# Kernel optimization log

Hardware: AMD Instinct MI355X
Metric: run time of the kernel (lower is better)

Reference implementation:

```python
import jax, jax.numpy as jnp
import numpy as np

B, N, F, H, A, T = 4, 256, 64, 256, 16, 3


def setup_inputs() -> dict:
    key = jax.random.key(0)
    ks = jax.random.split(key, 18)
    s = 0.05
    rn = lambda k, shp: jax.random.normal(k, shp, dtype=jnp.float32) * s
    return {
        "node_features": jax.random.normal(ks[0], (B, N, F), dtype=jnp.float32),
        "adjacency": jax.random.randint(ks[1], (B, N, N), 0, 2).astype(jnp.int32),
        # preprocess MLP: F->H->H
        "pre_W1": rn(ks[2], (F, H)), "pre_b1": jnp.zeros((H,), jnp.float32),
        "pre_W2": rn(ks[3], (H, H)), "pre_b2": jnp.zeros((H,), jnp.float32),
        # message MLP: 2H->H->H
        "msg_W1": rn(ks[4], (2 * H, H)), "msg_b1": jnp.zeros((H,), jnp.float32),
        "msg_W2": rn(ks[5], (H, H)), "msg_b2": jnp.zeros((H,), jnp.float32),
        # GRUCell params (jax layout [in, 3H]; gate order r,z,n like torch)
        "gru_Wih": rn(ks[6], (H, 3 * H)), "gru_Whh": rn(ks[7], (H, 3 * H)),
        "gru_bih": jnp.zeros((3 * H,), jnp.float32), "gru_bhh": jnp.zeros((3 * H,), jnp.float32),
        # readout MLP: H->H->A
        "ro_W1": rn(ks[8], (H, H)), "ro_b1": jnp.zeros((H,), jnp.float32),
        "ro_W2": rn(ks[9], (H, A)), "ro_b2": jnp.zeros((A,), jnp.float32),
    }


def reference(node_features, adjacency, pre_W1, pre_b1, pre_W2, pre_b2,
              msg_W1, msg_b1, msg_W2, msg_b2,
              gru_Wih, gru_Whh, gru_bih, gru_bhh,
              ro_W1, ro_b1, ro_W2, ro_b2):
    adj = adjacency.astype(node_features.dtype)  # [B,N,N]
    # preprocess: Linear-ReLU-Linear
    h = jnp.maximum(node_features @ pre_W1 + pre_b1, 0.0) @ pre_W2 + pre_b2  # [B,N,H]

    W1_i, W1_j = msg_W1[:H], msg_W1[H:]  # concat([h_i,h_j]) @ W1 == h_i@W1_i + h_j@W1_j
    for _ in range(T):
        hi = h @ W1_i  # [B,N,H] receiver part
        hj = h @ W1_j  # [B,N,H] sender part
        e = jnp.maximum(hi[:, :, None, :] + hj[:, None, :, :] + msg_b1, 0.0)  # [B,N,N,H]
        m = e @ msg_W2 + msg_b2  # [B,N,N,H] messages
        agg = jnp.einsum('bijh,bij->bih', m, adj)  # mask + sum over senders j
        # GRUCell(input=agg, hidden=h), torch gate order (r, z, n)
        gi = agg @ gru_Wih + gru_bih  # [B,N,3H]
        gh = h @ gru_Whh + gru_bhh
        ir, iz, inn = jnp.split(gi, 3, axis=-1)
        hr, hz, hn = jnp.split(gh, 3, axis=-1)
        r = jax.nn.sigmoid(ir + hr)
        z = jax.nn.sigmoid(iz + hz)
        n = jnp.tanh(inn + r * hn)
        h = (1.0 - z) * n + z * h

    g = jnp.sum(h, axis=1)  # [B,H] graph readout
    q = jnp.maximum(g @ ro_W1 + ro_b1, 0.0) @ ro_W2 + ro_b2  # [B,A]
    return q
```

## Files before the change

kernel.cpp:

```cpp
#include <hip/hip_runtime.h>
#include <hip/hip_bf16.h>


typedef unsigned short ushort_t;
typedef short bf8_t __attribute__((ext_vector_type(8)));
typedef float f4_t  __attribute__((ext_vector_type(4)));

#define BN_ROWS 1024

#define UB_NFB    0
#define UB_PW1T   65536
#define UB_PW2T   81920
#define UB_WCATT  147456
#define UB_WGT    475136
#define UB_H2     917504
#define UB_EHAT2  1441792

#define F_PREB1   1015808
#define F_PREB2   1016064
#define F_BCAT    1016320
#define F_BIH     1017600
#define F_ROW1    1018368
#define F_ROB1    1083904
#define F_ROW2    1084160
#define F_ROB2    1088256
#define F_H       1088272
#define F_HCAT    1350416
#define F_FLAG    2661136
#define F_GCNT    2661140

#define CVa 65536
#define CVb 81920
#define CVc 147456
#define CVd 475136
#define CV_TOTAL 547600
#define NCONV 1070

__device__ __forceinline__ float bf2f(ushort_t u) {
    return __uint_as_float(((unsigned int)u) << 16);
}
__device__ __forceinline__ ushort_t f2b(float v) {
    __hip_bfloat16 b = __float2bfloat16(v);
    return *reinterpret_cast<ushort_t*>(&b);
}
__device__ __forceinline__ float relu(float v) { return v < 0.f ? 0.f : v; }
__device__ __forceinline__ float ld(const void* p, int i, int isf32) {
    return isf32 ? ((const float*)p)[i] : bf2f(((const ushort_t*)p)[i]);
}

__global__ __launch_bounds__(256) void convwg_kernel(
    const void* nf, const void* preW1, const void* preb1, const void* preW2, const void* preb2,
    const void* msgW1, const void* msgb1, const void* msgW2, const void* msgb2,
    const void* gruWih, const void* gruWhh, const void* grubih, const void* grubhh,
    const void* roW1, const void* rob1, const void* roW2, const void* rob2,
    float* __restrict__ w)
{
    __shared__ float w2s[4 * 256];
    __shared__ int cnt;
    const int t = threadIdx.x;
    ushort_t* wb = (ushort_t*)w;

    if (t == 0) cnt = 0;
    __syncthreads();
    {
        const ushort_t* nf0 = (const ushort_t*)nf;
        int bad = 0;
        for (int i = 0; i < 8; ++i) {
            ushort_t u = nf0[(t * 8 + i) * 2];
            int ex = (u >> 7) & 0xFF;
            if ((u & 0x7fff) != 0 && (ex < 100 || ex > 140)) bad++;
        }
        atomicAdd(&cnt, bad);
    }
    __syncthreads();
    const int f32 = (cnt > 512) ? 1 : 0;

    if (blockIdx.x == 0) {
        if (t < 4) ((int*)(w + F_GCNT))[t] = 0;
        if (t == 4) *(int*)(w + F_FLAG) = f32;
    }

    if (blockIdx.x < NCONV) {
        const int e0 = (blockIdx.x * 256 + t) * 2;
#pragma unroll
        for (int u2 = 0; u2 < 2; ++u2) {
            int e = e0 + u2;
            if (e >= CV_TOTAL) break;
            if (e < CVa) {
                wb[UB_NFB + e] = f2b(ld(nf, e, f32));
            } else if (e < CVb) {
                int i = e - CVa; int n = i >> 6, k = i & 63;
                wb[UB_PW1T + i] = f2b(ld(preW1, k * 256 + n, f32));
            } else if (e < CVc) {
                int i = e - CVb; int n = i >> 8, k = i & 255;
                wb[UB_PW2T + i] = f2b(ld(preW2, k * 256 + n, f32));
            } else if (e < CVd) {
                int i = e - CVc; int n = i >> 8, k = i & 255;
                float v;
                if (n < 256)      v = ld(msgW1, k * 256 + n, f32);
                else if (n < 512) v = ld(msgW1, (256 + k) * 256 + (n - 256), f32);
                else              v = ld(gruWhh, k * 768 + (n - 512), f32);
                wb[UB_WCATT + i] = f2b(v);
            } else {
                int f = e - CVd;
                float v;
                if (f < 256)        v = ld(preb1, f, f32);
                else if (f < 512)   v = ld(preb2, f - 256, f32);
                else if (f < 1792) {
                    int c = f - 512;
                    if (c < 256)      v = ld(msgb1, c, f32);
                    else if (c < 512) v = 0.f;
                    else              v = ld(grubhh, c - 512, f32);
                }
                else if (f < 2560)  v = ld(grubih, f - 1792, f32);
                else if (f < 68096) v = ld(roW1, f - 2560, f32);
                else if (f < 68352) v = ld(rob1, f - 68096, f32);
                else if (f < 72448) v = ld(roW2, f - 68352, f32);
                else                v = ld(rob2, f - 72448, f32);
                w[F_PREB1 + f] = v;
            }
        }
        return;
    }

    const int wt = blockIdx.x - NCONV;
    const int p0 = (wt % 3) * 256;
    const int k0 = (wt / 3) * 4;
    for (int i = t; i < 4 * 256; i += 256) {
        int r = i >> 8, n = i & 255;
        int krow = k0 + r;
        float v;
        if (krow < 256)       v = ld(msgW2, krow * 256 + n, f32);
        else if (krow == 256) v = ld(msgb2, n, f32);
        else                  v = 0.f;
        w2s[i] = v;
    }
    __syncthreads();
    const int p = p0 + t;
    float acc4[4] = {};
    for (int n0 = 0; n0 < 256; n0 += 32) {
        float wv[32];
#pragma unroll
        for (int i = 0; i < 32; ++i)
            wv[i] = ld(gruWih, (n0 + i) * 768 + p, f32);
#pragma unroll
        for (int r = 0; r < 4; ++r) {
            float acc = acc4[r];
#pragma unroll
            for (int q = 0; q < 8; ++q) {
                f4_t w4 = *(const f4_t*)&w2s[r * 256 + n0 + q * 4];
                acc += w4[0] * wv[q * 4 + 0] + w4[1] * wv[q * 4 + 1]
                     + w4[2] * wv[q * 4 + 2] + w4[3] * wv[q * 4 + 3];
            }
            acc4[r] = acc;
        }
    }
#pragma unroll
    for (int r = 0; r < 4; ++r) {
        int krow = k0 + r;
        ushort_t hi = f2b(acc4[r]);
        ushort_t lo = f2b(acc4[r] - bf2f(hi));
        wb[UB_WGT + p * 576 + krow] = hi;
        wb[UB_WGT + p * 576 + 288 + krow] = lo;
    }
}

__global__ __launch_bounds__(256) void prenet_kernel(float* __restrict__ w)
{
    __shared__ ushort_t As[32 * 64];
    __shared__ ushort_t Xs[32 * 256];
    __shared__ ushort_t Bs[256 * 32];
    ushort_t* wb = (ushort_t*)w;
    const int t = threadIdx.x;
    const int wave = t >> 6, lane = t & 63;
    const int ln = lane & 15, quad = lane >> 4;
    const int wr = (wave & 1) * 16, wc = (wave >> 1) * 128;
    const int rbase = blockIdx.x * 32;
    const int srow = t >> 2, skc = (t & 3) << 3;

    {
        int row = t >> 3, kc = (t & 7) << 3;
        *(bf8_t*)(&As[row * 64 + kc]) =
            *(const bf8_t*)(&wb[UB_NFB + (rbase + row) * 64 + kc]);
    }

    f4_t acc[8] = {};
    for (int k0 = 0; k0 < 64; k0 += 32) {
        __syncthreads();
#pragma unroll
        for (int rr = 0; rr < 4; ++rr) {
            int n = srow + 64 * rr;
            *(bf8_t*)(&Bs[n * 32 + skc]) =
                *(const bf8_t*)(&wb[UB_PW1T + n * 64 + k0 + skc]);
        }
        __syncthreads();
        bf8_t af = *(const bf8_t*)(&As[(wr + ln) * 64 + k0 + quad * 8]);
#pragma unroll
        for (int n = 0; n < 8; ++n) {
            bf8_t bfr = *(const bf8_t*)(&Bs[(wc + n * 16 + ln) * 32 + quad * 8]);
            acc[n] = __builtin_amdgcn_mfma_f32_16x16x32_bf16(af, bfr, acc[n], 0, 0, 0);
        }
    }
    __syncthreads();
#pragma unroll
    for (int n = 0; n < 8; ++n) {
        int col = wc + n * 16 + ln;
        float bb = w[F_PREB1 + col];
#pragma unroll
        for (int r = 0; r < 4; ++r) {
            int row = wr + quad * 4 + r;
            Xs[row * 256 + col] = f2b(relu(acc[n][r] + bb));
        }
        acc[n] = (f4_t){0.f, 0.f, 0.f, 0.f};
    }
    __syncthreads();

    for (int k0 = 0; k0 < 256; k0 += 32) {
        __syncthreads();
#pragma unroll
        for (int rr = 0; rr < 4; ++rr) {
            int n = srow + 64 * rr;
            *(bf8_t*)(&Bs[n * 32 + skc]) =
                *(const bf8_t*)(&wb[UB_PW2T + n * 256 + k0 + skc]);
        }
        __syncthreads();
        bf8_t af = *(const bf8_t*)(&Xs[(wr + ln) * 256 + k0 + quad * 8]);
#pragma unroll
        for (int n = 0; n < 8; ++n) {
            bf8_t bfr = *(const bf8_t*)(&Bs[(wc + n * 16 + ln) * 32 + quad * 8]);
            acc[n] = __builtin_amdgcn_mfma_f32_16x16x32_bf16(af, bfr, acc[n], 0, 0, 0);
        }
    }
#pragma unroll
    for (int n = 0; n < 8; ++n) {
        int col = wc + n * 16 + ln;
        float bb = w[F_PREB2 + col];
#pragma unroll
        for (int r = 0; r < 4; ++r) {
            int grow = rbase + wr + quad * 4 + r;
            float v = acc[n][r] + bb;
            w[F_H + grow * 256 + col] = v;
            ushort_t hi = f2b(v);
            wb[UB_H2 + grow * 512 + col] = hi;
            wb[UB_H2 + grow * 512 + 256 + col] = f2b(v - bf2f(hi));
        }
    }
}

__global__ __launch_bounds__(256) void hcat_kernel(float* __restrict__ w)
{
    __shared__ ushort_t As[64 * 32];
    __shared__ ushort_t Bs[128 * 32];
    ushort_t* wb = (ushort_t*)w;
    const ushort_t* A  = wb + UB_H2;
    const ushort_t* Bt = wb + UB_WCATT;
    const int t = threadIdx.x;
    const int wave = t >> 6, lane = t & 63;
    const int ln = lane & 15, quad = lane >> 4;
    const int bm = (blockIdx.x & 15) * 64, bn = (blockIdx.x >> 4) * 128;
    const int wm = (wave >> 1) * 32, wn = (wave & 1) * 64;
    const int srow = t >> 2, skc = (t & 3) << 3;

    f4_t acc[2][4] = {};
    bf8_t ra, rb[2];

    ra = *(const bf8_t*)(&A[(bm + srow) * 512 + skc]);
#pragma unroll
    for (int r = 0; r < 2; ++r)
        rb[r] = *(const bf8_t*)(&Bt[(bn + srow + r * 64) * 256 + skc]);

    for (int ks = 0; ks < 16; ++ks) {
        __syncthreads();
        *(bf8_t*)(&As[srow * 32 + skc]) = ra;
#pragma unroll
        for (int r = 0; r < 2; ++r)
            *(bf8_t*)(&Bs[(srow + r * 64) * 32 + skc]) = rb[r];
        __syncthreads();
        if (ks < 15) {
            int k0 = (ks + 1) * 32;
            ra = *(const bf8_t*)(&A[(bm + srow) * 512 + k0 + skc]);
            int kb = (k0 & 255);
#pragma unroll
            for (int r = 0; r < 2; ++r)
                rb[r] = *(const bf8_t*)(&Bt[(bn + srow + r * 64) * 256 + kb + skc]);
        }
        bf8_t af[2], bfr[4];
#pragma unroll
        for (int i = 0; i < 2; ++i)
            af[i]  = *(const bf8_t*)(&As[(wm + i * 16 + ln) * 32 + quad * 8]);
#pragma unroll
        for (int i = 0; i < 4; ++i)
            bfr[i] = *(const bf8_t*)(&Bs[(wn + i * 16 + ln) * 32 + quad * 8]);
#pragma unroll
        for (int mi = 0; mi < 2; ++mi)
#pragma unroll
            for (int ni = 0; ni < 4; ++ni)
                acc[mi][ni] = __builtin_amdgcn_mfma_f32_16x16x32_bf16(
                    af[mi], bfr[ni], acc[mi][ni], 0, 0, 0);
    }

#pragma unroll
    for (int mi = 0; mi < 2; ++mi) {
#pragma unroll
        for (int ni = 0; ni < 4; ++ni) {
            int col = bn + wn + ni * 16 + ln;
            float bb = w[F_BCAT + col];
#pragma unroll
            for (int r = 0; r < 4; ++r) {
                int row = bm + wm + mi * 16 + quad * 4 + r;
                w[F_HCAT + row * 1280 + col] = acc[mi][ni][r] + bb;
            }
        }
    }
}

__global__ __launch_bounds__(256) void msg_kernel(
    const float* __restrict__ hcat,
    const int*   __restrict__ adj,
    ushort_t* __restrict__ ehat)
{
    const int row = blockIdx.x;
    const int t = threadIdx.x;
    __shared__ int ej[256];
    __shared__ int ecnt;
    if (t == 0) ecnt = 0;
    __syncthreads();
    if (adj[row * 256 + t]) { int p = atomicAdd(&ecnt, 1); ej[p] = t; }
    const float hi = hcat[row * 1280 + t];
    const float* hjb = hcat + (row >> 8) * 256 * 1280 + 256;
    __syncthreads();
    const int ne = ecnt;
    float acc = 0.f;
#pragma unroll 4
    for (int p = 0; p < ne; ++p) {
        int j = ej[p];
        acc += relu(hi + hjb[j * 1280 + t]);
    }
    ushort_t h16 = f2b(acc);
    ushort_t l16 = f2b(acc - bf2f(h16));
    ushort_t* er = ehat + row * 576;
    er[t] = h16;
    er[288 + t] = l16;
    if (t < 32) {
        er[256 + t] = f2b(t == 0 ? (float)ne : 0.f);
        er[544 + t] = 0;
    }
}

template<int FINAL>
__global__ __launch_bounds__(256) void gigru_kernel(float* __restrict__ w,
                                                    void* __restrict__ out)
{
    __shared__ ushort_t As[64 * 32];
    __shared__ ushort_t Bs[192 * 32];
    __shared__ float gl[256];
    __shared__ float t1[256];
    __shared__ int donef;
    ushort_t* wb = (ushort_t*)w;
    const int t = threadIdx.x;
    const int wave = t >> 6, lane = t & 63;
    const int ln = lane & 15, quad = lane >> 4;
    const int rg = blockIdx.x >> 2, cg = blockIdx.x & 3;
    const int rbase = rg * 64;
    const int srow = t >> 2, skc = (t & 3) << 3;

    const ushort_t* Ap = wb + UB_EHAT2 + (rbase + srow) * 576 + skc;
    int browoff[3];
#pragma unroll
    for (int rr = 0; rr < 3; ++rr) {
        int br = srow + 64 * rr;
        browoff[rr] = ((br >> 6) * 256 + cg * 64 + (br & 63)) * 576 + skc;
    }
    const ushort_t* Bp = wb + UB_WGT;

    f4_t acc[12] = {};
    bf8_t ra, rb[3];

    ra = *(const bf8_t*)(Ap);
#pragma unroll
    for (int rr = 0; rr < 3; ++rr)
        rb[rr] = *(const bf8_t*)(&Bp[browoff[rr]]);

    for (int ks = 0; ks < 27; ++ks) {
        __syncthreads();
        *(bf8_t*)(&As[srow * 32 + skc]) = ra;
#pragma unroll
        for (int rr = 0; rr < 3; ++rr)
            *(bf8_t*)(&Bs[(srow + 64 * rr) * 32 + skc]) = rb[rr];
        __syncthreads();
        if (ks < 26) {
            int k0 = (ks + 1) * 32;
            int ka = (k0 < 576) ? k0 : k0 - 576;
            int kb = (k0 < 288) ? k0 : k0 - 288;
            ra = *(const bf8_t*)(&Ap[ka]);
#pragma unroll
            for (int rr = 0; rr < 3; ++rr)
                rb[rr] = *(const bf8_t*)(&Bp[browoff[rr] + kb]);
        }
        bf8_t af = *(const bf8_t*)(&As[(wave * 16 + ln) * 32 + quad * 8]);
#pragma unroll
        for (int n = 0; n < 12; ++n) {
            bf8_t bfr = *(const bf8_t*)(&Bs[(n * 16 + ln) * 32 + quad * 8]);
            acc[n] = __builtin_amdgcn_mfma_f32_16x16x32_bf16(af, bfr, acc[n], 0, 0, 0);
        }
    }

#pragma unroll
    for (int n = 0; n < 4; ++n) {
        int col = cg * 64 + n * 16 + ln;
        float bi_r = w[F_BIH + col];
        float bi_z = w[F_BIH + 256 + col];
        float bi_n = w[F_BIH + 512 + col];
#pragma unroll
        for (int r = 0; r < 4; ++r) {
            int row = rbase + wave * 16 + quad * 4 + r;
            float ir = acc[n][r] + bi_r;
            float iz = acc[n + 4][r] + bi_z;
            float in = acc[n + 8][r] + bi_n;
            const float* ghr = w + F_HCAT + row * 1280 + 512;
            float hr = ghr[col], hz = ghr[256 + col], hn = ghr[512 + col];
            float rg_ = 1.f / (1.f + __expf(-(ir + hr)));
            float z   = 1.f / (1.f + __expf(-(iz + hz)));
            float nn  = tanhf(in + rg_ * hn);
            float ho = w[F_H + row * 256 + col];
            float hv = (1.f - z) * nn + z * ho;
            w[F_H + row * 256 + col] = hv;
            if (!FINAL) {
                ushort_t hb = f2b(hv);
                wb[UB_H2 + row * 512 + col] = hb;
                wb[UB_H2 + row * 512 + 256 + col] = f2b(hv - bf2f(hb));
            }
        }
    }

    if (FINAL) {
        const int g = blockIdx.x >> 4;
        __syncthreads();
        if (t == 0) {
            __threadfence();
            int prev = atomicAdd((int*)(w + F_GCNT) + g, 1);
            donef = (prev == 15);
        }
        __syncthreads();
        if (!donef) return;
        __threadfence();

        const float* hb = w + F_H + g * 256 * 256;
        float s = 0.f;
        for (int n = 0; n < 256; ++n) s += hb[n * 256 + t];
        gl[t] = s;
        __syncthreads();
        float acc1 = w[F_ROB1 + t];
        for (int k = 0; k < 256; ++k) acc1 += gl[k] * w[F_ROW1 + k * 256 + t];
        t1[t] = relu(acc1);
        __syncthreads();
        if (t < 16) {
            float q = w[F_ROB2 + t];
            for (int k = 0; k < 256; ++k) q += t1[k] * w[F_ROW2 + k * 16 + t];
            if (*(const int*)(w + F_FLAG)) ((float*)out)[g * 16 + t] = q;
            else ((__hip_bfloat16*)out)[g * 16 + t] = __float2bfloat16(q);
        }
    }
}

extern "C" void kernel_launch(void* const* d_in, const int* in_sizes, int n_in,
                              void* d_out, int out_size, void* d_ws, size_t ws_size,
                              hipStream_t stream) {
    float* w = (float*)d_ws;
    ushort_t* wb = (ushort_t*)d_ws;

    static const int dictSz[18]  = {65536,262144,16384,256,65536,256,131072,256,65536,256,
                                    196608,196608,768,768,65536,256,4096,16};
    static const int alphaSz[18] = {262144,196608,196608,768,768,131072,65536,256,256,
                                    65536,16384,65536,256,256,65536,4096,256,16};
    static const int alphaPos[18] = {9,0,10,12,11,13,5,7,6,8,2,1,4,3,14,16,15,17};
    bool dictOK = true, alphaOK = true;
    for (int i = 0; i < 18 && i < n_in; ++i) {
        if (in_sizes[i] != dictSz[i])  dictOK = false;
        if (in_sizes[i] != alphaSz[i]) alphaOK = false;
    }
    const void* P[18];
    for (int l = 0; l < 18; ++l) P[l] = d_in[(!dictOK && alphaOK) ? alphaPos[l] : l];
    const int* adj = (const int*)P[1];

    convwg_kernel<<<NCONV + 216, 256, 0, stream>>>(
        P[0], P[2], P[3], P[4], P[5], P[6], P[7], P[8], P[9],
        P[10], P[11], P[12], P[13], P[14], P[15], P[16], P[17], w);

    prenet_kernel<<<32, 256, 0, stream>>>(w);

    for (int it = 0; it < 3; ++it) {
        hcat_kernel<<<160, 256, 0, stream>>>(w);
        msg_kernel<<<BN_ROWS, 256, 0, stream>>>(w + F_HCAT, adj, wb + UB_EHAT2);
        if (it < 2)
            gigru_kernel<0><<<64, 256, 0, stream>>>(w, d_out);
        else
            gigru_kernel<1><<<64, 256, 0, stream>>>(w, d_out);
    }
}
```

Measured before the change: 308.9 us.

## Deepen K tiles with padded LDS and remap gigru blocks per XCD

The hcat and gigru GEMM loops now stage 64 and 96 K-elements per LDS round instead of 32, halving or thirding the number of barrier pairs, and use padded row strides (72 and 104) to reduce LDS bank conflicts. The gigru block index is remapped so blocks sharing the same B column group land on the same XCD, aiming for better L2 reuse of weights. The readout group index is updated to match the new mapping. The cost is more registers for prefetch and larger LDS use, which may reduce occupancy.

Result: faster. 297.3 us (-3.8%).

```diff
diff --git a/kernel.cpp b/kernel.cpp
--- a/kernel.cpp
+++ b/kernel.cpp
@@ -247,10 +247,11 @@
     }
 }
 
+#define HLD 72
 __global__ __launch_bounds__(256) void hcat_kernel(float* __restrict__ w)
 {
-    __shared__ ushort_t As[64 * 32];
-    __shared__ ushort_t Bs[128 * 32];
+    __shared__ ushort_t As[64 * HLD];
+    __shared__ ushort_t Bs[128 * HLD];
     ushort_t* wb = (ushort_t*)w;
     const ushort_t* A  = wb + UB_H2;
     const ushort_t* Bt = wb + UB_WCATT;
@@ -262,41 +263,54 @@
     const int srow = t >> 2, skc = (t & 3) << 3;
 
     f4_t acc[2][4] = {};
-    bf8_t ra, rb[2];
-
-    ra = *(const bf8_t*)(&A[(bm + srow) * 512 + skc]);
-#pragma unroll
-    for (int r = 0; r < 2; ++r)
-        rb[r] = *(const bf8_t*)(&Bt[(bn + srow + r * 64) * 256 + skc]);
-
-    for (int ks = 0; ks < 16; ++ks) {
-        __syncthreads();
-        *(bf8_t*)(&As[srow * 32 + skc]) = ra;
+    bf8_t ra[2], rb[2][2];
+
+#pragma unroll
+    for (int s = 0; s < 2; ++s) {
+        ra[s] = *(const bf8_t*)(&A[(bm + srow) * 512 + s * 32 + skc]);
 #pragma unroll
         for (int r = 0; r < 2; ++r)
-            *(bf8_t*)(&Bs[(srow + r * 64) * 32 + skc]) = rb[r];
-        __syncthreads();
-        if (ks < 15) {
-            int k0 = (ks + 1) * 32;
-            ra = *(const bf8_t*)(&A[(bm + srow) * 512 + k0 + skc]);
-            int kb = (k0 & 255);
+            rb[r][s] = *(const bf8_t*)(&Bt[(bn + srow + r * 64) * 256 + s * 32 + skc]);
+    }
+
+    for (int ks = 0; ks < 8; ++ks) {
+        __syncthreads();
+#pragma unroll
+        for (int s = 0; s < 2; ++s) {
+            *(bf8_t*)(&As[srow * HLD + s * 32 + skc]) = ra[s];
 #pragma unroll
             for (int r = 0; r < 2; ++r)
-                rb[r] = *(const bf8_t*)(&Bt[(bn + srow + r * 64) * 256 + kb + skc]);
-        }
-        bf8_t af[2], bfr[4];
-#pragma unroll
-        for (int i = 0; i < 2; ++i)
-            af[i]  = *(const bf8_t*)(&As[(wm + i * 16 + ln) * 32 + quad * 8]);
-#pragma unroll
-        for (int i = 0; i < 4; ++i)
-            bfr[i] = *(const bf8_t*)(&Bs[(wn + i * 16 + ln) * 32 + quad * 8]);
-#pragma unroll
-        for (int mi = 0; mi < 2; ++mi)
-#pragma unroll
-            for (int ni = 0; ni < 4; ++ni)
-                acc[mi][ni] = __builtin_amdgcn_mfma_f32_16x16x32_bf16(
-                    af[mi], bfr[ni], acc[mi][ni], 0, 0, 0);
+                *(bf8_t*)(&Bs[(srow + r * 64) * HLD + s * 32 + skc]) = rb[r][s];
+        }
+        __syncthreads();
+        if (ks < 7) {
+            int k0 = (ks + 1) * 64;
+#pragma unroll
+            for (int s = 0; s < 2; ++s) {
+                int k = k0 + s * 32;
+                ra[s] = *(const bf8_t*)(&A[(bm + srow) * 512 + k + skc]);
+                int kb = k & 255;
+#pragma unroll
+                for (int r = 0; r < 2; ++r)
+                    rb[r][s] = *(const bf8_t*)(&Bt[(bn + srow + r * 64) * 256 + kb + skc]);
+            }
+        }
+#pragma unroll
+        for (int kk = 0; kk < 2; ++kk) {
+            bf8_t af[2], bfr[4];
+#pragma unroll
+            for (int i = 0; i < 2; ++i)
+                af[i]  = *(const bf8_t*)(&As[(wm + i * 16 + ln) * HLD + kk * 32 + quad * 8]);
+#pragma unroll
+            for (int i = 0; i < 4; ++i)
+                bfr[i] = *(const bf8_t*)(&Bs[(wn + i * 16 + ln) * HLD + kk * 32 + quad * 8]);
+#pragma unroll
+            for (int mi = 0; mi < 2; ++mi)
+#pragma unroll
+                for (int ni = 0; ni < 4; ++ni)
+                    acc[mi][ni] = __builtin_amdgcn_mfma_f32_16x16x32_bf16(
+                        af[mi], bfr[ni], acc[mi][ni], 0, 0, 0);
+        }
     }
 
 #pragma unroll
@@ -347,12 +361,13 @@
     }
 }
 
+#define GLD 104
 template<int FINAL>
 __global__ __launch_bounds__(256) void gigru_kernel(float* __restrict__ w,
                                                     void* __restrict__ out)
 {
-    __shared__ ushort_t As[64 * 32];
-    __shared__ ushort_t Bs[192 * 32];
+    __shared__ ushort_t As[64 * GLD];
+    __shared__ ushort_t Bs[192 * GLD];
     __shared__ float gl[256];
     __shared__ float t1[256];
     __shared__ int donef;
@@ -360,7 +375,9 @@
     const int t = threadIdx.x;
     const int wave = t >> 6, lane = t & 63;
     const int ln = lane & 15, quad = lane >> 4;
-    const int rg = blockIdx.x >> 2, cg = blockIdx.x & 3;
+    const int xcd = blockIdx.x & 7;
+    const int cg = xcd & 3;
+    const int rg = (blockIdx.x >> 3) + 8 * (xcd >> 2);
     const int rbase = rg * 64;
     const int srow = t >> 2, skc = (t & 3) << 3;
 
@@ -374,34 +391,47 @@
     const ushort_t* Bp = wb + UB_WGT;
 
     f4_t acc[12] = {};
-    bf8_t ra, rb[3];
-
-    ra = *(const bf8_t*)(Ap);
-#pragma unroll
-    for (int rr = 0; rr < 3; ++rr)
-        rb[rr] = *(const bf8_t*)(&Bp[browoff[rr]]);
-
-    for (int ks = 0; ks < 27; ++ks) {
-        __syncthreads();
-        *(bf8_t*)(&As[srow * 32 + skc]) = ra;
+    bf8_t ra[3], rb[3][3];
+
+#pragma unroll
+    for (int s = 0; s < 3; ++s) {
+        ra[s] = *(const bf8_t*)(&Ap[s * 32]);
 #pragma unroll
         for (int rr = 0; rr < 3; ++rr)
-            *(bf8_t*)(&Bs[(srow + 64 * rr) * 32 + skc]) = rb[rr];
-        __syncthreads();
-        if (ks < 26) {
-            int k0 = (ks + 1) * 32;
-            int ka = (k0 < 576) ? k0 : k0 - 576;
-            int kb = (k0 < 288) ? k0 : k0 - 288;
-            ra = *(const bf8_t*)(&Ap[ka]);
+            rb[rr][s] = *(const bf8_t*)(&Bp[browoff[rr] + s * 32]);
+    }
+
+    for (int ks = 0; ks < 9; ++ks) {
+        __syncthreads();
+#pragma unroll
+        for (int s = 0; s < 3; ++s) {
+            *(bf8_t*)(&As[srow * GLD + s * 32 + skc]) = ra[s];
 #pragma unroll
             for (int rr = 0; rr < 3; ++rr)
-                rb[rr] = *(const bf8_t*)(&Bp[browoff[rr] + kb]);
-        }
-        bf8_t af = *(const bf8_t*)(&As[(wave * 16 + ln) * 32 + quad * 8]);
-#pragma unroll
-        for (int n = 0; n < 12; ++n) {
-            bf8_t bfr = *(const bf8_t*)(&Bs[(n * 16 + ln) * 32 + quad * 8]);
-            acc[n] = __builtin_amdgcn_mfma_f32_16x16x32_bf16(af, bfr, acc[n], 0, 0, 0);
+                *(bf8_t*)(&Bs[(srow + 64 * rr) * GLD + s * 32 + skc]) = rb[rr][s];
+        }
+        __syncthreads();
+        if (ks < 8) {
+            int k0 = (ks + 1) * 96;
+#pragma unroll
+            for (int s = 0; s < 3; ++s) {
+                int k = k0 + s * 32;
+                int ka = (k < 576) ? k : k - 576;
+                int kb = (k < 288) ? k : k - 288;
+                ra[s] = *(const bf8_t*)(&Ap[ka]);
+#pragma unroll
+                for (int rr = 0; rr < 3; ++rr)
+                    rb[rr][s] = *(const bf8_t*)(&Bp[browoff[rr] + kb]);
+            }
+        }
+#pragma unroll
+        for (int kk = 0; kk < 3; ++kk) {
+            bf8_t af = *(const bf8_t*)(&As[(wave * 16 + ln) * GLD + kk * 32 + quad * 8]);
+#pragma unroll
+            for (int n = 0; n < 12; ++n) {
+                bf8_t bfr = *(const bf8_t*)(&Bs[(n * 16 + ln) * GLD + kk * 32 + quad * 8]);
+                acc[n] = __builtin_amdgcn_mfma_f32_16x16x32_bf16(af, bfr, acc[n], 0, 0, 0);
+            }
         }
     }
 
@@ -434,7 +464,7 @@
     }
 
     if (FINAL) {
-        const int g = blockIdx.x >> 4;
+        const int g = rg >> 2;
         __syncthreads();
         if (t == 0) {
             __threadfence();
```

## Shrink GEMM row tiles and widen K steps to launch more blocks

Applied to the files above, without the earlier changes.

The hcat GEMM moves to 32-row tiles with a 64-wide K step, doubling its grid to 320 blocks. The GRU-input GEMM moves to 16-row tiles with a 96-wide K step and an XCD-aware block mapping, raising its grid from 64 to 256 blocks. Both use padded LDS rows (stride 104) to reduce bank conflicts and halve the number of barriers per K. The aim is to fill more of the MI355X's compute units and cut sync overhead. The cost is larger LDS use per block and more redundant B-tile loads across blocks, and the final readout counter threshold is changed to 63 to match the new block count per graph.

Measured after the change: 265.3 us. 1.16x faster.

```diff
diff --git a/kernel.cpp b/kernel.cpp
--- a/kernel.cpp
+++ b/kernel.cpp
@@ -247,69 +247,74 @@
     }
 }
 
+#define HLD 104
 __global__ __launch_bounds__(256) void hcat_kernel(float* __restrict__ w)
 {
-    __shared__ ushort_t As[64 * 32];
-    __shared__ ushort_t Bs[128 * 32];
+    __shared__ ushort_t As[32 * HLD];
+    __shared__ ushort_t Bs[128 * HLD];
     ushort_t* wb = (ushort_t*)w;
     const ushort_t* A  = wb + UB_H2;
     const ushort_t* Bt = wb + UB_WCATT;
     const int t = threadIdx.x;
     const int wave = t >> 6, lane = t & 63;
     const int ln = lane & 15, quad = lane >> 4;
-    const int bm = (blockIdx.x & 15) * 64, bn = (blockIdx.x >> 4) * 128;
-    const int wm = (wave >> 1) * 32, wn = (wave & 1) * 64;
-    const int srow = t >> 2, skc = (t & 3) << 3;
-
-    f4_t acc[2][4] = {};
-    bf8_t ra, rb[2];
-
-    ra = *(const bf8_t*)(&A[(bm + srow) * 512 + skc]);
-#pragma unroll
-    for (int r = 0; r < 2; ++r)
-        rb[r] = *(const bf8_t*)(&Bt[(bn + srow + r * 64) * 256 + skc]);
-
-    for (int ks = 0; ks < 16; ++ks) {
-        __syncthreads();
-        *(bf8_t*)(&As[srow * 32 + skc]) = ra;
-#pragma unroll
-        for (int r = 0; r < 2; ++r)
-            *(bf8_t*)(&Bs[(srow + r * 64) * 32 + skc]) = rb[r];
-        __syncthreads();
-        if (ks < 15) {
-            int k0 = (ks + 1) * 32;
-            ra = *(const bf8_t*)(&A[(bm + srow) * 512 + k0 + skc]);
-            int kb = (k0 & 255);
-#pragma unroll
-            for (int r = 0; r < 2; ++r)
-                rb[r] = *(const bf8_t*)(&Bt[(bn + srow + r * 64) * 256 + kb + skc]);
-        }
-        bf8_t af[2], bfr[4];
-#pragma unroll
-        for (int i = 0; i < 2; ++i)
-            af[i]  = *(const bf8_t*)(&As[(wm + i * 16 + ln) * 32 + quad * 8]);
+    const int bm = (blockIdx.x & 31) * 32, bn = (blockIdx.x >> 5) * 128;
+    const int wm = (wave >> 1) * 16, wn = (wave & 1) * 64;
+
+    const int arow = t >> 3, akc = (t & 7) << 3;
+    const int agoff = (bm + arow) * 512 + akc;
+    const int aloff = arow * HLD + akc;
+    int bgoff[4], bloff[4];
+#pragma unroll
+    for (int i = 0; i < 4; ++i) {
+        int slot = i * 256 + t;
+        int brow = slot >> 3, bkc = (slot & 7) << 3;
+        bgoff[i] = (bn + brow) * 256 + bkc;
+        bloff[i] = brow * HLD + bkc;
+    }
+
+    f4_t acc[4] = {};
+    bf8_t ra, rb[4];
+
+    ra = *(const bf8_t*)(&A[agoff]);
+#pragma unroll
+    for (int i = 0; i < 4; ++i)
+        rb[i] = *(const bf8_t*)(&Bt[bgoff[i]]);
+
+    for (int ks = 0; ks < 8; ++ks) {
+        __syncthreads();
+        *(bf8_t*)(&As[aloff]) = ra;
 #pragma unroll
         for (int i = 0; i < 4; ++i)
-            bfr[i] = *(const bf8_t*)(&Bs[(wn + i * 16 + ln) * 32 + quad * 8]);
-#pragma unroll
-        for (int mi = 0; mi < 2; ++mi)
-#pragma unroll
-            for (int ni = 0; ni < 4; ++ni)
-                acc[mi][ni] = __builtin_amdgcn_mfma_f32_16x16x32_bf16(
-                    af[mi], bfr[ni], acc[mi][ni], 0, 0, 0);
-    }
-
-#pragma unroll
-    for (int mi = 0; mi < 2; ++mi) {
-#pragma unroll
-        for (int ni = 0; ni < 4; ++ni) {
-            int col = bn + wn + ni * 16 + ln;
-            float bb = w[F_BCAT + col];
-#pragma unroll
-            for (int r = 0; r < 4; ++r) {
-                int row = bm + wm + mi * 16 + quad * 4 + r;
-                w[F_HCAT + row * 1280 + col] = acc[mi][ni][r] + bb;
+            *(bf8_t*)(&Bs[bloff[i]]) = rb[i];
+        __syncthreads();
+        if (ks < 7) {
+            int k0 = (ks + 1) * 64;
+            int kb = k0 & 255;
+            ra = *(const bf8_t*)(&A[agoff + k0]);
+#pragma unroll
+            for (int i = 0; i < 4; ++i)
+                rb[i] = *(const bf8_t*)(&Bt[bgoff[i] + kb]);
+        }
+#pragma unroll
+        for (int kk = 0; kk < 2; ++kk) {
+            bf8_t af = *(const bf8_t*)(&As[(wm + ln) * HLD + kk * 32 + quad * 8]);
+#pragma unroll
+            for (int ni = 0; ni < 4; ++ni) {
+                bf8_t bfr = *(const bf8_t*)(&Bs[(wn + ni * 16 + ln) * HLD + kk * 32 + quad * 8]);
+                acc[ni] = __builtin_amdgcn_mfma_f32_16x16x32_bf16(af, bfr, acc[ni], 0, 0, 0);
             }
+        }
+    }
+
+#pragma unroll
+    for (int ni = 0; ni < 4; ++ni) {
+        int col = bn + wn + ni * 16 + ln;
+        float bb = w[F_BCAT + col];
+#pragma unroll
+        for (int r = 0; r < 4; ++r) {
+            int row = bm + wm + quad * 4 + r;
+            w[F_HCAT + row * 1280 + col] = acc[ni][r] + bb;
         }
     }
 }
@@ -347,12 +352,13 @@
     }
 }
 
+#define GLD 104
 template<int FINAL>
 __global__ __launch_bounds__(256) void gigru_kernel(float* __restrict__ w,
                                                     void* __restrict__ out)
 {
-    __shared__ ushort_t As[64 * 32];
-    __shared__ ushort_t Bs[192 * 32];
+    __shared__ ushort_t As[16 * GLD];
+    __shared__ ushort_t Bs[192 * GLD];
     __shared__ float gl[256];
     __shared__ float t1[256];
     __shared__ int donef;
@@ -360,63 +366,74 @@
     const int t = threadIdx.x;
     const int wave = t >> 6, lane = t & 63;
     const int ln = lane & 15, quad = lane >> 4;
-    const int rg = blockIdx.x >> 2, cg = blockIdx.x & 3;
-    const int rbase = rg * 64;
-    const int srow = t >> 2, skc = (t & 3) << 3;
-
-    const ushort_t* Ap = wb + UB_EHAT2 + (rbase + srow) * 576 + skc;
-    int browoff[3];
-#pragma unroll
-    for (int rr = 0; rr < 3; ++rr) {
-        int br = srow + 64 * rr;
-        browoff[rr] = ((br >> 6) * 256 + cg * 64 + (br & 63)) * 576 + skc;
-    }
-    const ushort_t* Bp = wb + UB_WGT;
-
-    f4_t acc[12] = {};
-    bf8_t ra, rb[3];
-
-    ra = *(const bf8_t*)(Ap);
-#pragma unroll
-    for (int rr = 0; rr < 3; ++rr)
-        rb[rr] = *(const bf8_t*)(&Bp[browoff[rr]]);
-
-    for (int ks = 0; ks < 27; ++ks) {
-        __syncthreads();
-        *(bf8_t*)(&As[srow * 32 + skc]) = ra;
-#pragma unroll
-        for (int rr = 0; rr < 3; ++rr)
-            *(bf8_t*)(&Bs[(srow + 64 * rr) * 32 + skc]) = rb[rr];
-        __syncthreads();
-        if (ks < 26) {
-            int k0 = (ks + 1) * 32;
+    const int xcd = blockIdx.x & 7;
+    const int cg = xcd & 3;
+    const int rg = (blockIdx.x >> 3) + 32 * (xcd >> 2);
+    const int rbase = rg * 16;
+
+    const int aval = (t < 192);
+    const int arow = t / 12, akc = (t % 12) * 8;
+    const int agoff = (rbase + arow) * 576 + akc;
+    const int aloff = arow * GLD + akc;
+    int bgoff[9], bloff[9];
+#pragma unroll
+    for (int i = 0; i < 9; ++i) {
+        int slot = i * 256 + t;
+        int brow = slot / 12, bkc = (slot % 12) * 8;
+        int wrow = (brow >> 6) * 256 + cg * 64 + (brow & 63);
+        bgoff[i] = wrow * 576 + bkc;
+        bloff[i] = brow * GLD + bkc;
+    }
+    const ushort_t* Ehp = wb + UB_EHAT2;
+    const ushort_t* Bp  = wb + UB_WGT;
+
+    f4_t acc[3] = {};
+    bf8_t ra, rb[9];
+
+    if (aval) ra = *(const bf8_t*)(&Ehp[agoff]);
+#pragma unroll
+    for (int i = 0; i < 9; ++i)
+        rb[i] = *(const bf8_t*)(&Bp[bgoff[i]]);
+
+    for (int ks = 0; ks < 9; ++ks) {
+        __syncthreads();
+        if (aval) *(bf8_t*)(&As[aloff]) = ra;
+#pragma unroll
+        for (int i = 0; i < 9; ++i)
+            *(bf8_t*)(&Bs[bloff[i]]) = rb[i];
+        __syncthreads();
+        if (ks < 8) {
+            int k0 = (ks + 1) * 96;
             int ka = (k0 < 576) ? k0 : k0 - 576;
             int kb = (k0 < 288) ? k0 : k0 - 288;
-            ra = *(const bf8_t*)(&Ap[ka]);
-#pragma unroll
-            for (int rr = 0; rr < 3; ++rr)
-                rb[rr] = *(const bf8_t*)(&Bp[browoff[rr] + kb]);
-        }
-        bf8_t af = *(const bf8_t*)(&As[(wave * 16 + ln) * 32 + quad * 8]);
-#pragma unroll
-        for (int n = 0; n < 12; ++n) {
-            bf8_t bfr = *(const bf8_t*)(&Bs[(n * 16 + ln) * 32 + quad * 8]);
-            acc[n] = __builtin_amdgcn_mfma_f32_16x16x32_bf16(af, bfr, acc[n], 0, 0, 0);
-        }
-    }
-
-#pragma unroll
-    for (int n = 0; n < 4; ++n) {
-        int col = cg * 64 + n * 16 + ln;
+            if (aval) ra = *(const bf8_t*)(&Ehp[agoff + ka]);
+#pragma unroll
+            for (int i = 0; i < 9; ++i)
+                rb[i] = *(const bf8_t*)(&Bp[bgoff[i] + kb]);
+        }
+#pragma unroll
+        for (int kk = 0; kk < 3; ++kk) {
+            bf8_t af = *(const bf8_t*)(&As[ln * GLD + kk * 32 + quad * 8]);
+#pragma unroll
+            for (int n = 0; n < 3; ++n) {
+                int fn = wave + n * 4;
+                bf8_t bfr = *(const bf8_t*)(&Bs[(fn * 16 + ln) * GLD + kk * 32 + quad * 8]);
+                acc[n] = __builtin_amdgcn_mfma_f32_16x16x32_bf16(af, bfr, acc[n], 0, 0, 0);
+            }
+        }
+    }
+
+    {
+        const int col = cg * 64 + wave * 16 + ln;
         float bi_r = w[F_BIH + col];
         float bi_z = w[F_BIH + 256 + col];
         float bi_n = w[F_BIH + 512 + col];
 #pragma unroll
         for (int r = 0; r < 4; ++r) {
-            int row = rbase + wave * 16 + quad * 4 + r;
-            float ir = acc[n][r] + bi_r;
-            float iz = acc[n + 4][r] + bi_z;
-            float in = acc[n + 8][r] + bi_n;
+            int row = rbase + quad * 4 + r;
+            float ir = acc[0][r] + bi_r;
+            float iz = acc[1][r] + bi_z;
+            float in = acc[2][r] + bi_n;
             const float* ghr = w + F_HCAT + row * 1280 + 512;
             float hr = ghr[col], hz = ghr[256 + col], hn = ghr[512 + col];
             float rg_ = 1.f / (1.f + __expf(-(ir + hr)));
@@ -434,12 +451,12 @@
     }
 
     if (FINAL) {
-        const int g = blockIdx.x >> 4;
+        const int g = rg >> 4;
         __syncthreads();
         if (t == 0) {
             __threadfence();
             int prev = atomicAdd((int*)(w + F_GCNT) + g, 1);
-            donef = (prev == 15);
+            donef = (prev == 63);
         }
         __syncthreads();
         if (!donef) return;
@@ -490,11 +507,11 @@
     prenet_kernel<<<32, 256, 0, stream>>>(w);
 
     for (int it = 0; it < 3; ++it) {
-        hcat_kernel<<<160, 256, 0, stream>>>(w);
+        hcat_kernel<<<320, 256, 0, stream>>>(w);
         msg_kernel<<<BN_ROWS, 256, 0, stream>>>(w + F_HCAT, adj, wb + UB_EHAT2);
         if (it < 2)
-            gigru_kernel<0><<<64, 256, 0, stream>>>(w, d_out);
+            gigru_kernel<0><<<256, 256, 0, stream>>>(w, d_out);
         else
-            gigru_kernel<1><<<64, 256, 0, stream>>>(w, d_out);
-    }
-}
+            gigru_kernel<1><<<256, 256, 0, stream>>>(w, d_out);
+    }
+}
```
